# Performance work log

Hardware: AMD Instinct MI355X
Metric: run time of the kernel (lower is better)

The kernel has to match this reference:

```python
import jax, jax.numpy as jnp
import numpy as np

B, T, QD, KD, AD = 64, 2048, 512, 512, 512
SCALING = 1.0
NEG = -1e10


def setup_inputs() -> dict:
    key = jax.random.key(0)
    ks = jax.random.split(key, 10)
    s = 0.02
    return {
        "query": jax.random.normal(ks[0], (B, QD), jnp.float32),
        "keys": jax.random.normal(ks[1], (B, T, KD), jnp.float32),
        "value": jax.random.normal(ks[2], (B, T, KD), jnp.float32),
        "cover": jax.random.uniform(ks[3], (B, T), jnp.float32),
        "key_len": jax.random.randint(ks[4], (B,), T // 2, T + 1),
        "Wq": jax.random.normal(ks[5], (QD, AD), jnp.float32) * s,
        "bq": jnp.zeros((AD,), jnp.float32),
        "Wk": jax.random.normal(ks[6], (KD, AD), jnp.float32) * s,
        "Wc": jax.random.normal(ks[7], (1, AD), jnp.float32) * s,
        "Wo": jax.random.normal(ks[8], (AD, 1), jnp.float32) * s,
    }


def reference(query, keys, value, cover, key_len, Wq, bq, Wk, Wc, Wo):
    # projections
    q = query @ Wq + bq                      # [B, A]
    k = jnp.einsum("btd,da->bta", keys, Wk)  # [B, T, A]
    c = cover[..., None] * Wc[0]             # [B, T, A]  (Linear(1, A), no bias)
    # additive energy
    e = jnp.tanh(q[:, None, :] + k + c)      # [B, T, A]
    energy = jnp.einsum("bta,ao->bot", e, Wo)  # [B, 1, T]
    # mask padded positions (t >= key_len)
    mask = jnp.arange(T)[None, None, :] >= key_len[:, None, None]  # [B, 1, T]
    energy = jnp.where(mask, NEG, energy)
    attn = jax.nn.softmax(energy * SCALING, axis=2)  # [B, 1, T]
    context = jnp.einsum("bqt,btd->bqd", attn, value)[:, 0, :]  # [B, KD]
    return context, attn
```

## Files before the change

### kernel.cpp

```cpp
#include <hip/hip_runtime.h>
#include <hip/hip_bf16.h>

#define B_ 64
#define T_ 2048
#define D_ 512
#define A_ 512
#define BM 128
#define BN 128
#define BK 32
#define NSTEP (D_/BK)

typedef float f32x4_t __attribute__((ext_vector_type(4)));
typedef short bf16x8_t __attribute__((ext_vector_type(8)));

#define GLL16(g, l) __builtin_amdgcn_global_load_lds( \
    (const __attribute__((address_space(1))) void*)(g), \
    (__attribute__((address_space(3))) void*)(l), 16, 0, 0)

__global__ void __launch_bounds__(256) qproj_kernel(
    const float* __restrict__ query, const float* __restrict__ Wq,
    const float* __restrict__ bq, float* __restrict__ qbuf) {
  __shared__ float qs[D_];
  const int b = blockIdx.x, tid = threadIdx.x;
  qs[tid] = query[b*D_ + tid];
  qs[tid+256] = query[b*D_ + tid + 256];
  __syncthreads();
  float a0 = bq[tid], a1 = bq[tid+256];
  for (int d = 0; d < D_; ++d) {
    const float qv = qs[d];
    a0 += qv * Wq[d*A_ + tid];
    a1 += qv * Wq[d*A_ + tid + 256];
  }
  qbuf[b*A_ + tid] = a0;
  qbuf[b*A_ + tid+256] = a1;
}

__global__ void __launch_bounds__(256) wkprep_kernel(
    const float* __restrict__ Wk, unsigned int* __restrict__ slab) {
  __shared__ float tile[32][65];
  const int kb = blockIdx.x >> 3;
  const int a0 = (blockIdx.x & 7) * 64;
  const int tid = threadIdx.x;
  for (int p = 0; p < 8; ++p) {
    const int idx = p*256 + tid;
    const int k = idx >> 6, al = idx & 63;
    tile[k][al] = Wk[(kb*32 + k)*A_ + a0 + al];
  }
  __syncthreads();
  const int al = tid >> 2, c = tid & 3;
  const int a = a0 + al;
  union { __hip_bfloat162 h[2]; uint2 u; } w0, w1;
  w0.h[0] = __float22bfloat162_rn(make_float2(tile[c*8+0][al], tile[c*8+1][al]));
  w0.h[1] = __float22bfloat162_rn(make_float2(tile[c*8+2][al], tile[c*8+3][al]));
  w1.h[0] = __float22bfloat162_rn(make_float2(tile[c*8+4][al], tile[c*8+5][al]));
  w1.h[1] = __float22bfloat162_rn(make_float2(tile[c*8+6][al], tile[c*8+7][al]));
  const int cpos = c ^ ((a >> 1) & 3);
  *(uint4*)(slab + (kb*512 + a)*16 + cpos*4) =
      make_uint4(w0.u.x, w0.u.y, w1.u.x, w1.u.y);
}

__global__ void __launch_bounds__(256, 3) energy_kernel(
    const float* __restrict__ keys, const float* __restrict__ cover,
    const int* __restrict__ key_len, const unsigned char* __restrict__ slab,
    const float* __restrict__ qbuf, const float* __restrict__ Wc,
    const float* __restrict__ Wo, float* __restrict__ epart) {
  __shared__ __align__(16) unsigned char Abuf[3][BM*64];
  __shared__ __align__(16) unsigned char Bbuf[3][BN*64];
  __shared__ float redbuf[4][64];

  const int d = blockIdx.x;
  const int logical = (d & 7) * 512 + (d >> 3);
  const int ct = logical & 3;
  const int tt = (logical >> 2) & 15;
  const int b  = logical >> 6;

  const int t0 = tt * BM;
  const int kl = key_len[b];
  if (t0 >= kl) return;

  const int tid = threadIdx.x;
  const int wid = tid >> 6;
  const int lane = tid & 63;
  const int lq = lane >> 4, lr = lane & 15;
  const int wm = wid >> 1, wn = wid & 1;

  const int sr = tid >> 1, sh = tid & 1;
  const float* agp = keys + ((size_t)b*T_ + t0 + sr)*D_ + sh*16;
  const int sx = (sr >> 1) & 3;
  const int sw0 = sr*64 + (((2*sh + 0) ^ sx) << 4);
  const int sw1 = sr*64 + (((2*sh + 1) ^ sx) << 4);

  const unsigned char* bsl = slab + ct*8192 + wid*1024 + lane*16;

  f32x4_t acc[4][4];
  #pragma unroll
  for (int i = 0; i < 4; ++i)
    #pragma unroll
    for (int j = 0; j < 4; ++j) acc[i][j] = 0.0f;

  int a_off[4], b_off[4];
  #pragma unroll
  for (int mf = 0; mf < 4; ++mf) {
    const int r = wm*64 + mf*16 + lr;
    a_off[mf] = r*64 + ((lq ^ ((r >> 1) & 3)) << 4);
  }
  #pragma unroll
  for (int nf = 0; nf < 4; ++nf) {
    const int r = wn*64 + nf*16 + lr;
    b_off[nf] = r*64 + ((lq ^ ((r >> 1) & 3)) << 4);
  }

  f32x4_t pA[4];
  auto agload = [&](int ksrc) {
    const float* p = agp + ksrc*BK;
    pA[0] = *(const f32x4_t*)(p);
    pA[1] = *(const f32x4_t*)(p + 4);
    pA[2] = *(const f32x4_t*)(p + 8);
    pA[3] = *(const f32x4_t*)(p + 12);
  };
  auto bgll = [&](int ksrc, unsigned char* Bdst) {
    const unsigned char* g = bsl + (size_t)ksrc*32768;
    GLL16(g,        Bdst + wid*1024);
    GLL16(g + 4096, Bdst + 4096 + wid*1024);
  };
  auto apack = [&](unsigned char* Adst) {
    union { __hip_bfloat162 h[2]; uint2 u; } q0, q1;
    q0.h[0] = __float22bfloat162_rn(make_float2(pA[0][0], pA[0][1]));
    q0.h[1] = __float22bfloat162_rn(make_float2(pA[0][2], pA[0][3]));
    q1.h[0] = __float22bfloat162_rn(make_float2(pA[1][0], pA[1][1]));
    q1.h[1] = __float22bfloat162_rn(make_float2(pA[1][2], pA[1][3]));
    *(uint4*)(Adst + sw0) = make_uint4(q0.u.x, q0.u.y, q1.u.x, q1.u.y);
    q0.h[0] = __float22bfloat162_rn(make_float2(pA[2][0], pA[2][1]));
    q0.h[1] = __float22bfloat162_rn(make_float2(pA[2][2], pA[2][3]));
    q1.h[0] = __float22bfloat162_rn(make_float2(pA[3][0], pA[3][1]));
    q1.h[1] = __float22bfloat162_rn(make_float2(pA[3][2], pA[3][3]));
    *(uint4*)(Adst + sw1) = make_uint4(q0.u.x, q0.u.y, q1.u.x, q1.u.y);
  };

  unsigned char *Ar = Abuf[0], *An = Abuf[1], *Aw = Abuf[2];
  unsigned char *Br = Bbuf[0], *Bn = Bbuf[1], *Bw = Bbuf[2];

  agload(0); bgll(0, Br);
  apack(Ar);
  agload(1); bgll(1, Bn);
  apack(An);
  asm volatile("s_waitcnt lgkmcnt(0)" ::: "memory");
  __builtin_amdgcn_s_barrier();
  __builtin_amdgcn_sched_barrier(0);

  for (int ks = 0; ks < NSTEP; ++ks) {
    const bool pre = (ks + 2 < NSTEP);
    if (pre) {
      agload(ks + 2);
      bgll(ks + 2, Bw);
    }
    bf16x8_t aF[4], bF[4];
    #pragma unroll
    for (int mf = 0; mf < 4; ++mf) aF[mf] = *(const bf16x8_t*)(Ar + a_off[mf]);
    #pragma unroll
    for (int nf = 0; nf < 4; ++nf) bF[nf] = *(const bf16x8_t*)(Br + b_off[nf]);
    #pragma unroll
    for (int mf = 0; mf < 4; ++mf)
      #pragma unroll
      for (int nf = 0; nf < 4; ++nf)
        acc[mf][nf] = __builtin_amdgcn_mfma_f32_16x16x32_bf16(aF[mf], bF[nf], acc[mf][nf], 0, 0, 0);
    if (pre) apack(Aw);
    if (ks + 1 < NSTEP) {
      if (!pre)
        asm volatile("s_waitcnt vmcnt(0)" ::: "memory");
      asm volatile("s_waitcnt lgkmcnt(0)" ::: "memory");
      __builtin_amdgcn_s_barrier();
      __builtin_amdgcn_sched_barrier(0);
    }
    unsigned char* t;
    t = Ar; Ar = An; An = Aw; Aw = t;
    t = Br; Br = Bn; Bn = Bw; Bw = t;
  }

  float cov[4][4];
  #pragma unroll
  for (int mf = 0; mf < 4; ++mf)
    #pragma unroll
    for (int j = 0; j < 4; ++j)
      cov[mf][j] = cover[(size_t)b*T_ + t0 + wm*64 + mf*16 + lq*4 + j];

  float ep[4][4];
  #pragma unroll
  for (int mf = 0; mf < 4; ++mf)
    #pragma unroll
    for (int j = 0; j < 4; ++j) ep[mf][j] = 0.f;

  #pragma unroll
  for (int nf = 0; nf < 4; ++nf) {
    const int n = ct*BN + wn*64 + nf*16 + lr;
    const float qv = qbuf[b*A_ + n];
    const float wc = Wc[n];
    const float wo = Wo[n];
    #pragma unroll
    for (int mf = 0; mf < 4; ++mf)
      #pragma unroll
      for (int j = 0; j < 4; ++j) {
        float p = acc[mf][nf][j] + qv + cov[mf][j] * wc;
        p = fminf(fmaxf(p, -15.f), 15.f);
        const float t2 = __expf(2.f * p);
        ep[mf][j] += wo * ((t2 - 1.f) * __builtin_amdgcn_rcpf(t2 + 1.f));
      }
  }
  #pragma unroll
  for (int mf = 0; mf < 4; ++mf)
    #pragma unroll
    for (int j = 0; j < 4; ++j) {
      float v = ep[mf][j];
      v += __shfl_xor(v, 1); v += __shfl_xor(v, 2);
      v += __shfl_xor(v, 4); v += __shfl_xor(v, 8);
      ep[mf][j] = v;
    }
  if (lr == 0) {
    #pragma unroll
    for (int mf = 0; mf < 4; ++mf)
      #pragma unroll
      for (int j = 0; j < 4; ++j)
        redbuf[wid][mf*16 + lq*4 + j] = ep[mf][j];
  }
  __syncthreads();
  if (tid < BM) {
    const int wmm = tid >> 6, rl = tid & 63;
    epart[((size_t)ct*B_ + b)*T_ + t0 + tid] = redbuf[wmm*2][rl] + redbuf[wmm*2+1][rl];
  }
}

__global__ void __launch_bounds__(1024) softmax_kernel(
    const float* __restrict__ epart, const int* __restrict__ key_len,
    float* __restrict__ attn) {
  __shared__ float sredM[16];
  __shared__ float sredS[16];
  const int b = blockIdx.x, tid = threadIdx.x;
  const int kl = key_len[b];
  float e0 = -3.0e38f, e1 = -3.0e38f;
  if (tid < kl)
    e0 = epart[(size_t)b*T_ + tid] + epart[((size_t)B_ + b)*T_ + tid]
       + epart[((size_t)2*B_ + b)*T_ + tid] + epart[((size_t)3*B_ + b)*T_ + tid];
  if (tid + 1024 < kl)
    e1 = epart[(size_t)b*T_ + tid+1024] + epart[((size_t)B_ + b)*T_ + tid+1024]
       + epart[((size_t)2*B_ + b)*T_ + tid+1024] + epart[((size_t)3*B_ + b)*T_ + tid+1024];
  float m = fmaxf(e0, e1);
  for (int s = 32; s; s >>= 1) m = fmaxf(m, __shfl_xor(m, s));
  if ((tid & 63) == 0) sredM[tid >> 6] = m;
  __syncthreads();
  float M = -3.0e38f;
  #pragma unroll
  for (int i = 0; i < 16; ++i) M = fmaxf(M, sredM[i]);
  const float p0 = (tid < kl) ? __expf(e0 - M) : 0.f;
  const float p1 = (tid + 1024 < kl) ? __expf(e1 - M) : 0.f;
  float s = p0 + p1;
  for (int k = 32; k; k >>= 1) s += __shfl_xor(s, k);
  if ((tid & 63) == 0) sredS[tid >> 6] = s;
  __syncthreads();
  float S = 0.f;
  #pragma unroll
  for (int i = 0; i < 16; ++i) S += sredS[i];
  const float inv = 1.f / S;
  attn[b*T_ + tid] = p0 * inv;
  attn[b*T_ + tid + 1024] = p1 * inv;
}

__global__ void __launch_bounds__(256) ctxpart_kernel(
    const float* __restrict__ value, const float* __restrict__ attn,
    const int* __restrict__ key_len, float* __restrict__ partial) {
  __shared__ float att_s[256];
  const int b = blockIdx.y, ch = blockIdx.x;
  const int tid = threadIdx.x;
  const int kl = key_len[b];
  const int tstart = ch * 256;
  const int tend = min(256, kl - tstart);
  float ax = 0.f, ay = 0.f;
  if (tend > 0) {
    att_s[tid] = attn[b*T_ + tstart + tid];
    __syncthreads();
    const float2* vp = (const float2*)(value + ((size_t)b*T_ + tstart)*D_) + tid;
    #pragma unroll 4
    for (int i = 0; i < tend; ++i) {
      const float w = att_s[i];
      const float2 v = vp[(size_t)i * 256];
      ax += w * v.x; ay += w * v.y;
    }
  }
  float2* pp = (float2*)(partial + (size_t)(b*8 + ch)*D_) + tid;
  *pp = make_float2(ax, ay);
}

__global__ void __launch_bounds__(256) ctxsum_kernel(
    const float* __restrict__ partial, float* __restrict__ ctx) {
  const int b = blockIdx.x, tid = threadIdx.x;
  float sx = 0.f, sy = 0.f;
  #pragma unroll
  for (int c = 0; c < 8; ++c) {
    const float2 v = *((const float2*)(partial + (size_t)(b*8 + c)*D_) + tid);
    sx += v.x; sy += v.y;
  }
  *((float2*)(ctx + (size_t)b*D_) + tid) = make_float2(sx, sy);
}

extern "C" void kernel_launch(void* const* d_in, const int* in_sizes, int n_in,
                              void* d_out, int out_size, void* d_ws, size_t ws_size,
                              hipStream_t stream) {
  const float* query  = (const float*)d_in[0];
  const float* keys   = (const float*)d_in[1];
  const float* value  = (const float*)d_in[2];
  const float* cover  = (const float*)d_in[3];
  const int*   key_len= (const int*)d_in[4];
  const float* Wq     = (const float*)d_in[5];
  const float* bq     = (const float*)d_in[6];
  const float* Wk     = (const float*)d_in[7];
  const float* Wc     = (const float*)d_in[8];
  const float* Wo     = (const float*)d_in[9];

  float* out = (float*)d_out;
  float* ctx_out  = out;
  float* attn_out = out + B_*A_;

  float* ws = (float*)d_ws;
  float* qbuf    = ws;
  float* epart   = ws + 32768;
  float* partial = ws + 32768 + 524288;
  unsigned int* slab = (unsigned int*)(ws + 32768 + 524288 + 262144);

  qproj_kernel<<<B_, 256, 0, stream>>>(query, Wq, bq, qbuf);
  wkprep_kernel<<<128, 256, 0, stream>>>(Wk, slab);
  energy_kernel<<<B_*(T_/BM)*(A_/BN), 256, 0, stream>>>(
      keys, cover, key_len, (const unsigned char*)slab, qbuf, Wc, Wo, epart);
  softmax_kernel<<<B_, 1024, 0, stream>>>(epart, key_len, attn_out);
  ctxpart_kernel<<<dim3(8, B_), 256, 0, stream>>>(value, attn_out, key_len, partial);
  ctxsum_kernel<<<B_, 256, 0, stream>>>(partial, ctx_out);
}
```

Measured before the change: 239.8 us.

## Pre-convert keys to bf16 slab and stream both GEMM operands via direct LDS loads

Adds a pre-pass kernel that converts keys to bf16 in a K-blocked layout in workspace. The energy GEMM can then load both A and B tiles with global_load_lds, with no register staging or in-loop conversion. The swizzle moves from the stored slab into the per-thread load address. Before, each of the four column-tile blocks reread the fp32 keys; now keys are read in fp32 once and the GEMM reads half the bytes. The cost is an extra 128 MB workspace write plus read. A fallback kernel keeps the old path when the workspace is too small.

```diff
diff --git a/kernel.cpp b/kernel.cpp
--- a/kernel.cpp
+++ b/kernel.cpp
@@ -54,14 +54,38 @@
   w0.h[1] = __float22bfloat162_rn(make_float2(tile[c*8+2][al], tile[c*8+3][al]));
   w1.h[0] = __float22bfloat162_rn(make_float2(tile[c*8+4][al], tile[c*8+5][al]));
   w1.h[1] = __float22bfloat162_rn(make_float2(tile[c*8+6][al], tile[c*8+7][al]));
-  const int cpos = c ^ ((a >> 1) & 3);
-  *(uint4*)(slab + (kb*512 + a)*16 + cpos*4) =
+  *(uint4*)(slab + (kb*512 + a)*16 + c*4) =
       make_uint4(w0.u.x, w0.u.y, w1.u.x, w1.u.y);
 }
 
+__global__ void __launch_bounds__(256) kprep_kernel(
+    const float* __restrict__ keys, const int* __restrict__ key_len,
+    unsigned int* __restrict__ kslabA) {
+  const int b = blockIdx.y;
+  const int tt2 = blockIdx.x;
+  if (tt2 * 16 >= key_len[b]) return;
+  const int tid = threadIdx.x;
+  const int tl = tid >> 4, kb = tid & 15;
+  const int t = tt2*16 + tl;
+  const float* src = keys + ((size_t)b*T_ + t)*D_ + kb*32;
+  f32x4_t v[8];
+  #pragma unroll
+  for (int j = 0; j < 8; ++j) v[j] = *(const f32x4_t*)(src + j*4);
+  unsigned int* dst = kslabA + ((size_t)(b*16 + kb)*T_ + t)*16;
+  #pragma unroll
+  for (int c = 0; c < 4; ++c) {
+    union { __hip_bfloat162 h[2]; uint2 u; } w0, w1;
+    w0.h[0] = __float22bfloat162_rn(make_float2(v[2*c][0],   v[2*c][1]));
+    w0.h[1] = __float22bfloat162_rn(make_float2(v[2*c][2],   v[2*c][3]));
+    w1.h[0] = __float22bfloat162_rn(make_float2(v[2*c+1][0], v[2*c+1][1]));
+    w1.h[1] = __float22bfloat162_rn(make_float2(v[2*c+1][2], v[2*c+1][3]));
+    *(uint4*)(dst + c*4) = make_uint4(w0.u.x, w0.u.y, w1.u.x, w1.u.y);
+  }
+}
+
 __global__ void __launch_bounds__(256, 3) energy_kernel(
-    const float* __restrict__ keys, const float* __restrict__ cover,
-    const int* __restrict__ key_len, const unsigned char* __restrict__ slab,
+    const unsigned char* __restrict__ kslabA, const float* __restrict__ cover,
+    const int* __restrict__ key_len, const unsigned char* __restrict__ slabB,
     const float* __restrict__ qbuf, const float* __restrict__ Wc,
     const float* __restrict__ Wo, float* __restrict__ epart) {
   __shared__ __align__(16) unsigned char Abuf[3][BM*64];
@@ -84,13 +108,158 @@
   const int lq = lane >> 4, lr = lane & 15;
   const int wm = wid >> 1, wn = wid & 1;
 
+  const int sr = tid >> 2, ss = tid & 3;
+  const int soff = sr*64 + ((ss ^ ((sr >> 1) & 3)) << 4);
+  const unsigned char* asrc = kslabA + ((size_t)b*16*T_ + t0)*64 + soff;
+  const unsigned char* bsrc = slabB + (size_t)ct*128*64 + soff;
+
+  f32x4_t acc[4][4];
+  #pragma unroll
+  for (int i = 0; i < 4; ++i)
+    #pragma unroll
+    for (int j = 0; j < 4; ++j) acc[i][j] = 0.0f;
+
+  int a_off[4], b_off[4];
+  #pragma unroll
+  for (int mf = 0; mf < 4; ++mf) {
+    const int r = wm*64 + mf*16 + lr;
+    a_off[mf] = r*64 + ((lq ^ ((r >> 1) & 3)) << 4);
+  }
+  #pragma unroll
+  for (int nf = 0; nf < 4; ++nf) {
+    const int r = wn*64 + nf*16 + lr;
+    b_off[nf] = r*64 + ((lq ^ ((r >> 1) & 3)) << 4);
+  }
+
+  unsigned char *Ar = Abuf[0], *An = Abuf[1], *Aw = Abuf[2];
+  unsigned char *Br = Bbuf[0], *Bn = Bbuf[1], *Bw = Bbuf[2];
+
+  auto stage = [&](int ks, unsigned char* Ad, unsigned char* Bd) {
+    const unsigned char* Ag = asrc + (size_t)ks * (T_*64);
+    GLL16(Ag,        Ad + wid*1024);
+    GLL16(Ag + 4096, Ad + 4096 + wid*1024);
+    const unsigned char* Bg = bsrc + (size_t)ks * 32768;
+    GLL16(Bg,        Bd + wid*1024);
+    GLL16(Bg + 4096, Bd + 4096 + wid*1024);
+  };
+
+  stage(0, Ar, Br);
+  stage(1, An, Bn);
+  asm volatile("s_waitcnt vmcnt(4)" ::: "memory");
+  __builtin_amdgcn_s_barrier();
+  __builtin_amdgcn_sched_barrier(0);
+
+  #pragma unroll 1
+  for (int ks = 0; ks < NSTEP; ++ks) {
+    if (ks + 2 < NSTEP) stage(ks + 2, Aw, Bw);
+    bf16x8_t aF[4], bF[4];
+    #pragma unroll
+    for (int mf = 0; mf < 4; ++mf) aF[mf] = *(const bf16x8_t*)(Ar + a_off[mf]);
+    #pragma unroll
+    for (int nf = 0; nf < 4; ++nf) bF[nf] = *(const bf16x8_t*)(Br + b_off[nf]);
+    #pragma unroll
+    for (int mf = 0; mf < 4; ++mf)
+      #pragma unroll
+      for (int nf = 0; nf < 4; ++nf)
+        acc[mf][nf] = __builtin_amdgcn_mfma_f32_16x16x32_bf16(aF[mf], bF[nf], acc[mf][nf], 0, 0, 0);
+    if (ks + 1 < NSTEP) {
+      if (ks + 2 < NSTEP)
+        asm volatile("s_waitcnt vmcnt(4)" ::: "memory");
+      else
+        asm volatile("s_waitcnt vmcnt(0)" ::: "memory");
+      __builtin_amdgcn_s_barrier();
+      __builtin_amdgcn_sched_barrier(0);
+    }
+    unsigned char* t;
+    t = Ar; Ar = An; An = Aw; Aw = t;
+    t = Br; Br = Bn; Bn = Bw; Bw = t;
+  }
+
+  float cov[4][4];
+  #pragma unroll
+  for (int mf = 0; mf < 4; ++mf)
+    #pragma unroll
+    for (int j = 0; j < 4; ++j)
+      cov[mf][j] = cover[(size_t)b*T_ + t0 + wm*64 + mf*16 + lq*4 + j];
+
+  float ep[4][4];
+  #pragma unroll
+  for (int mf = 0; mf < 4; ++mf)
+    #pragma unroll
+    for (int j = 0; j < 4; ++j) ep[mf][j] = 0.f;
+
+  #pragma unroll
+  for (int nf = 0; nf < 4; ++nf) {
+    const int n = ct*BN + wn*64 + nf*16 + lr;
+    const float qv = qbuf[b*A_ + n];
+    const float wc = Wc[n];
+    const float wo = Wo[n];
+    #pragma unroll
+    for (int mf = 0; mf < 4; ++mf)
+      #pragma unroll
+      for (int j = 0; j < 4; ++j) {
+        float p = acc[mf][nf][j] + qv + cov[mf][j] * wc;
+        p = fminf(fmaxf(p, -15.f), 15.f);
+        const float t2 = __expf(2.f * p);
+        ep[mf][j] += wo * ((t2 - 1.f) * __builtin_amdgcn_rcpf(t2 + 1.f));
+      }
+  }
+  #pragma unroll
+  for (int mf = 0; mf < 4; ++mf)
+    #pragma unroll
+    for (int j = 0; j < 4; ++j) {
+      float v = ep[mf][j];
+      v += __shfl_xor(v, 1); v += __shfl_xor(v, 2);
+      v += __shfl_xor(v, 4); v += __shfl_xor(v, 8);
+      ep[mf][j] = v;
+    }
+  if (lr == 0) {
+    #pragma unroll
+    for (int mf = 0; mf < 4; ++mf)
+      #pragma unroll
+      for (int j = 0; j < 4; ++j)
+        redbuf[wid][mf*16 + lq*4 + j] = ep[mf][j];
+  }
+  __syncthreads();
+  if (tid < BM) {
+    const int wmm = tid >> 6, rl = tid & 63;
+    epart[((size_t)ct*B_ + b)*T_ + t0 + tid] = redbuf[wmm*2][rl] + redbuf[wmm*2+1][rl];
+  }
+}
+
+__global__ void __launch_bounds__(256, 3) energy_fb_kernel(
+    const float* __restrict__ keys, const float* __restrict__ cover,
+    const int* __restrict__ key_len, const unsigned char* __restrict__ slabB,
+    const float* __restrict__ qbuf, const float* __restrict__ Wc,
+    const float* __restrict__ Wo, float* __restrict__ epart) {
+  __shared__ __align__(16) unsigned char Abuf[3][BM*64];
+  __shared__ __align__(16) unsigned char Bbuf[3][BN*64];
+  __shared__ float redbuf[4][64];
+
+  const int d = blockIdx.x;
+  const int logical = (d & 7) * 512 + (d >> 3);
+  const int ct = logical & 3;
+  const int tt = (logical >> 2) & 15;
+  const int b  = logical >> 6;
+  const int t0 = tt * BM;
+  const int kl = key_len[b];
+  if (t0 >= kl) return;
+
+  const int tid = threadIdx.x;
+  const int wid = tid >> 6;
+  const int lane = tid & 63;
+  const int lq = lane >> 4, lr = lane & 15;
+  const int wm = wid >> 1, wn = wid & 1;
+
   const int sr = tid >> 1, sh = tid & 1;
   const float* agp = keys + ((size_t)b*T_ + t0 + sr)*D_ + sh*16;
   const int sx = (sr >> 1) & 3;
   const int sw0 = sr*64 + (((2*sh + 0) ^ sx) << 4);
   const int sw1 = sr*64 + (((2*sh + 1) ^ sx) << 4);
 
-  const unsigned char* bsl = slab + ct*8192 + wid*1024 + lane*16;
+  const int ssr = tid >> 2, sss = tid & 3;
+  const int soff = ssr*64 + ((sss ^ ((ssr >> 1) & 3)) << 4);
+  const unsigned char* bsrc = slabB + (size_t)ct*128*64 + soff;
 
   f32x4_t acc[4][4];
   #pragma unroll
@@ -119,7 +288,7 @@
     pA[3] = *(const f32x4_t*)(p + 12);
   };
   auto bgll = [&](int ksrc, unsigned char* Bdst) {
-    const unsigned char* g = bsl + (size_t)ksrc*32768;
+    const unsigned char* g = bsrc + (size_t)ksrc*32768;
     GLL16(g,        Bdst + wid*1024);
     GLL16(g + 4096, Bdst + 4096 + wid*1024);
   };
@@ -140,20 +309,15 @@
   unsigned char *Ar = Abuf[0], *An = Abuf[1], *Aw = Abuf[2];
   unsigned char *Br = Bbuf[0], *Bn = Bbuf[1], *Bw = Bbuf[2];
 
-  agload(0); bgll(0, Br);
-  apack(Ar);
-  agload(1); bgll(1, Bn);
-  apack(An);
+  agload(0); bgll(0, Br); apack(Ar);
+  agload(1); bgll(1, Bn); apack(An);
   asm volatile("s_waitcnt lgkmcnt(0)" ::: "memory");
   __builtin_amdgcn_s_barrier();
   __builtin_amdgcn_sched_barrier(0);
 
   for (int ks = 0; ks < NSTEP; ++ks) {
     const bool pre = (ks + 2 < NSTEP);
-    if (pre) {
-      agload(ks + 2);
-      bgll(ks + 2, Bw);
-    }
+    if (pre) { agload(ks + 2); bgll(ks + 2, Bw); }
     bf16x8_t aF[4], bF[4];
     #pragma unroll
     for (int mf = 0; mf < 4; ++mf) aF[mf] = *(const bf16x8_t*)(Ar + a_off[mf]);
@@ -166,8 +330,7 @@
         acc[mf][nf] = __builtin_amdgcn_mfma_f32_16x16x32_bf16(aF[mf], bF[nf], acc[mf][nf], 0, 0, 0);
     if (pre) apack(Aw);
     if (ks + 1 < NSTEP) {
-      if (!pre)
-        asm volatile("s_waitcnt vmcnt(0)" ::: "memory");
+      if (!pre) asm volatile("s_waitcnt vmcnt(0)" ::: "memory");
       asm volatile("s_waitcnt lgkmcnt(0)" ::: "memory");
       __builtin_amdgcn_s_barrier();
       __builtin_amdgcn_sched_barrier(0);
@@ -183,13 +346,11 @@
     #pragma unroll
     for (int j = 0; j < 4; ++j)
       cov[mf][j] = cover[(size_t)b*T_ + t0 + wm*64 + mf*16 + lq*4 + j];
-
   float ep[4][4];
   #pragma unroll
   for (int mf = 0; mf < 4; ++mf)
     #pragma unroll
     for (int j = 0; j < 4; ++j) ep[mf][j] = 0.f;
-
   #pragma unroll
   for (int nf = 0; nf < 4; ++nf) {
     const int n = ct*BN + wn*64 + nf*16 + lr;
@@ -319,16 +480,26 @@
   float* ctx_out  = out;
   float* attn_out = out + B_*A_;
 
-  float* ws = (float*)d_ws;
-  float* qbuf    = ws;
-  float* epart   = ws + 32768;
-  float* partial = ws + 32768 + 524288;
-  unsigned int* slab = (unsigned int*)(ws + 32768 + 524288 + 262144);
+  char* ws = (char*)d_ws;
+  float* qbuf    = (float*)ws;
+  float* epart   = (float*)(ws + 131072);
+  float* partial = (float*)(ws + 131072 + 2097152);
+  unsigned int* slabB = (unsigned int*)(ws + 131072 + 2097152 + 1048576);
+  const size_t small_end = 131072 + 2097152 + 1048576 + 524288;
+  unsigned int* kslabA = (unsigned int*)(ws + small_end);
+  const size_t need = small_end + 134217728ull;
 
   qproj_kernel<<<B_, 256, 0, stream>>>(query, Wq, bq, qbuf);
-  wkprep_kernel<<<128, 256, 0, stream>>>(Wk, slab);
-  energy_kernel<<<B_*(T_/BM)*(A_/BN), 256, 0, stream>>>(
-      keys, cover, key_len, (const unsigned char*)slab, qbuf, Wc, Wo, epart);
+  wkprep_kernel<<<128, 256, 0, stream>>>(Wk, slabB);
+  if (ws_size >= need) {
+    kprep_kernel<<<dim3(T_/16, B_), 256, 0, stream>>>(keys, key_len, kslabA);
+    energy_kernel<<<B_*(T_/BM)*(A_/BN), 256, 0, stream>>>(
+        (const unsigned char*)kslabA, cover, key_len, (const unsigned char*)slabB,
+        qbuf, Wc, Wo, epart);
+  } else {
+    energy_fb_kernel<<<B_*(T_/BM)*(A_/BN), 256, 0, stream>>>(
+        keys, cover, key_len, (const unsigned char*)slabB, qbuf, Wc, Wo, epart);
+  }
   softmax_kernel<<<B_, 1024, 0, stream>>>(epart, key_len, attn_out);
   ctxpart_kernel<<<dim3(8, B_), 256, 0, stream>>>(value, attn_out, key_len, partial);
   ctxsum_kernel<<<B_, 256, 0, stream>>>(partial, ctx_out);
```

New measurement: 242.0 us. No clear change (+0.9%).
